# Kernel optimization log

Hardware: AMD Instinct MI355X
Metric: run time of the kernel (lower is better)

Reference implementation:

```python
import jax, jax.numpy as jnp
import numpy as np

N = 1_000_000
HID = 128

def setup_inputs() -> dict:
    key = jax.random.key(0)
    ks = jax.random.split(key, 4)
    F = jnp.eye(2, dtype=jnp.float32)[None] + 0.1 * jax.random.normal(ks[0], (N, 2, 2), dtype=jnp.float32)
    W1 = jax.random.normal(ks[1], (7, HID), dtype=jnp.float32) * (1.0 / np.sqrt(7))
    b1 = jnp.zeros((HID,), dtype=jnp.float32)
    W2 = jax.random.normal(ks[2], (HID, HID), dtype=jnp.float32) * (1.0 / np.sqrt(HID))
    b2 = jnp.zeros((HID,), dtype=jnp.float32)
    W3 = jax.random.normal(ks[3], (HID, 4), dtype=jnp.float32) * (1.0 / np.sqrt(HID))
    b3 = jnp.zeros((4,), dtype=jnp.float32)
    return {"F": F, "W1": W1, "b1": b1, "W2": W2, "b2": b2, "W3": W3, "b3": b3}

def reference(F, W1, b1, W2, b2, W3, b3):
    F = F.reshape(-1, 2, 2)                      # [N,2,2]
    U, sigma, Vh = jnp.linalg.svd(F)             # batched 2x2 SVD
    R = jnp.matmul(U, Vh)                        # rotation part, [N,2,2]
    FtF = jnp.einsum('nij,nik->njk', F, F)       # F^T F, [N,2,2]
    I = jnp.eye(2, dtype=F.dtype)
    I1 = sigma - 1.0                             # [N,2]
    I2 = (FtF - I).reshape(-1, 4)                # [N,4]
    det = F[:, 0, 0] * F[:, 1, 1] - F[:, 0, 1] * F[:, 1, 0]
    I3 = det[:, None] - 1.0                      # [N,1]
    inv = jnp.concatenate([I1, I2, I3], axis=1)  # [N,7]
    h = jax.nn.relu(inv @ W1 + b1)
    h = jax.nn.relu(h @ W2 + b2)
    x = (h @ W3 + b3).reshape(-1, 2, 2)
    x = (x + jnp.swapaxes(x, 1, 2)) * 0.5        # symmetrize
    delta_Fp = jnp.matmul(R, x)
    return delta_Fp + F
```

## Files before the change

kernel.cpp:

```cpp
#include <hip/hip_runtime.h>

typedef _Float16 f16x8 __attribute__((ext_vector_type(8)));
typedef _Float16 f16x2 __attribute__((ext_vector_type(2)));
typedef float    f32x4 __attribute__((ext_vector_type(4)));

#define MFMA(a, b, c) __builtin_amdgcn_mfma_f32_16x16x32_f16((a), (b), (c), 0, 0, 0)

__device__ inline f16x8 zero8() {
    f16x8 z;
#pragma unroll
    for (int i = 0; i < 8; ++i) z[i] = (_Float16)0.0f;
    return z;
}

__global__ __launch_bounds__(256, 1)
void DeformationCorrector_78967268704761_kernel(
        const float* __restrict__ F,
        const float* __restrict__ W1, const float* __restrict__ b1,
        const float* __restrict__ W2, const float* __restrict__ b2,
        const float* __restrict__ W3, const float* __restrict__ b3,
        float* __restrict__ out, int N)
{
    __shared__ __align__(16) _Float16 W2f[8][4][64][8];
    __shared__ __align__(16) _Float16 W1f[8][16][8];
    __shared__ __align__(16) _Float16 W3c[4][16][8];
    __shared__ __align__(16) _Float16 invL[256][8];
    __shared__ __align__(16) _Float16 scratch[4][64][40];

    const int tid  = threadIdx.x;
    const int lane = tid & 63;
    const int w    = tid >> 6;
    const int l15  = tid & 15;
    const int quad = (tid >> 4) & 3;

    for (int m = tid; m < 128 * 128; m += 256) {
        int k = m >> 7, n = m & 127;
        W2f[n >> 4][k >> 5][((k >> 3) & 3) * 16 + (n & 15)][k & 7] = (_Float16)W2[m];
    }
    for (int f = tid; f < 1024; f += 256) {
        int nt = f >> 7, n15 = (f >> 3) & 15, j = f & 7;
        W1f[nt][n15][j] = (_Float16)((j < 7) ? W1[j * 128 + nt * 16 + n15]
                                             : b1[nt * 16 + n15]);
    }
    for (int f = tid; f < 512; f += 256) {
        int s = f >> 7, idx = (f >> 3) & 15, j = f & 7;
        int q = idx >> 2, n = idx & 3;
        W3c[s][idx][j] = (_Float16)W3[(s * 32 + q * 8 + j) * 4 + n];
    }
    float b2r[8];
#pragma unroll
    for (int nt = 0; nt < 8; ++nt) b2r[nt] = b2[nt * 16 + l15];
    const float b3v = (l15 < 4) ? b3[l15] : 0.f;
    __syncthreads();

    const int ntiles = (N + 255) >> 8;
    for (int tile = blockIdx.x; tile < ntiles; tile += (int)gridDim.x) {
        const int p = tile * 256 + tid;

        float a, b, c, d;
        if (p < N) {
            const float4 f4 = *(const float4*)(F + 4ll * p);
            a = f4.x; b = f4.y; c = f4.z; d = f4.w;
        } else { a = 1.f; b = 0.f; c = 0.f; d = 1.f; }
        const float x1 = a + d, y1 = c - b, x2 = a - d, y2 = c + b;
        const float h1v = sqrtf(x1 * x1 + y1 * y1);
        const float h2v = sqrtf(x2 * x2 + y2 * y2);
        const float s1 = 0.5f * (h1v + h2v), s2 = 0.5f * (h1v - h2v);
        const float ir = 1.0f / h1v;
        const float Rc = x1 * ir, Rs = y1 * ir;
        f16x8 iv;
        iv[0] = (_Float16)(s1 - 1.f);
        iv[1] = (_Float16)(s2 - 1.f);
        iv[2] = (_Float16)(a * a + c * c - 1.f);
        const float i3 = a * b + c * d;
        iv[3] = (_Float16)i3;
        iv[4] = (_Float16)i3;
        iv[5] = (_Float16)(b * b + d * d - 1.f);
        iv[6] = (_Float16)(a * d - b * c - 1.f);
        iv[7] = (_Float16)1.0f;
        *(f16x8*)(&invL[tid][0]) = iv;

        f16x8 binv[4];
#pragma unroll
        for (int mt = 0; mt < 4; ++mt)
            binv[mt] = (quad == 0) ? *(const f16x8*)(&invL[w * 64 + mt * 16 + l15][0])
                                   : zero8();

        f32x4 acc2[8][4];
#pragma unroll
        for (int nt2 = 0; nt2 < 8; ++nt2)
#pragma unroll
            for (int mt2 = 0; mt2 < 4; ++mt2) acc2[nt2][mt2] = (f32x4){0.f, 0.f, 0.f, 0.f};

        for (int ks = 0; ks < 4; ++ks) {
#pragma unroll
            for (int h = 0; h < 2; ++h) {
                const f16x8 bw1 = (lane < 16) ? *(const f16x8*)(&W1f[2 * ks + h][l15][0])
                                              : zero8();
#pragma unroll
                for (int mt = 0; mt < 4; ++mt) {
                    f32x4 cz = {0.f, 0.f, 0.f, 0.f};
                    const f32x4 cc = MFMA(binv[mt], bw1, cz);
#pragma unroll
                    for (int r = 0; r < 4; ++r)
                        scratch[w][mt * 16 + quad * 4 + r][h * 16 + l15] =
                            (_Float16)fmaxf(cc[r], 0.f);
                }
            }
            f16x8 af[4];
#pragma unroll
            for (int mt2 = 0; mt2 < 4; ++mt2)
                af[mt2] = *(const f16x8*)(&scratch[w][mt2 * 16 + l15][quad * 8]);
#pragma unroll
            for (int nt2 = 0; nt2 < 8; ++nt2) {
                const f16x8 bf = *(const f16x8*)(&W2f[nt2][ks][lane][0]);
#pragma unroll
                for (int mt2 = 0; mt2 < 4; ++mt2)
                    acc2[nt2][mt2] = MFMA(af[mt2], bf, acc2[nt2][mt2]);
            }
        }

        f32x4 acc3[4];
#pragma unroll
        for (int mt2 = 0; mt2 < 4; ++mt2) acc3[mt2] = (f32x4){0.f, 0.f, 0.f, 0.f};

#pragma unroll
        for (int s = 0; s < 4; ++s) {
#pragma unroll
            for (int h = 0; h < 2; ++h) {
                const int nt2 = 2 * s + h;
                const float bb = b2r[nt2];
#pragma unroll
                for (int mt2 = 0; mt2 < 4; ++mt2)
#pragma unroll
                    for (int r = 0; r < 4; ++r)
                        scratch[w][mt2 * 16 + quad * 4 + r][h * 16 + l15] =
                            (_Float16)fmaxf(acc2[nt2][mt2][r] + bb, 0.f);
            }
            const f16x8 bw3 = (l15 < 4) ? *(const f16x8*)(&W3c[s][quad * 4 + l15][0])
                                        : zero8();
#pragma unroll
            for (int mt2 = 0; mt2 < 4; ++mt2) {
                const f16x8 ah = *(const f16x8*)(&scratch[w][mt2 * 16 + l15][quad * 8]);
                acc3[mt2] = MFMA(ah, bw3, acc3[mt2]);
            }
        }

        float* xf = (float*)(&scratch[w][0][0]);
#pragma unroll
        for (int mt2 = 0; mt2 < 4; ++mt2)
#pragma unroll
            for (int r = 0; r < 4; ++r)
                if (l15 < 4)
                    xf[(mt2 * 16 + quad * 4 + r) * 4 + l15] = acc3[mt2][r] + b3v;

        const float4 xv = *(const float4*)(&xf[lane * 4]);
        const float xm  = 0.5f * (xv.y + xv.z);
        const float d00 = Rc * xv.x - Rs * xm;
        const float d01 = Rc * xm   - Rs * xv.w;
        const float d10 = Rs * xv.x + Rc * xm;
        const float d11 = Rs * xm   + Rc * xv.w;
        if (p < N) {
            float4 o;
            o.x = a + d00; o.y = b + d01; o.z = c + d10; o.w = d + d11;
            *(float4*)(out + 4ll * p) = o;
        }
    }
}

extern "C" void kernel_launch(void* const* d_in, const int* in_sizes, int n_in,
                              void* d_out, int out_size, void* d_ws, size_t ws_size,
                              hipStream_t stream) {
    const float* F  = (const float*)d_in[0];
    const float* W1 = (const float*)d_in[1];
    const float* b1 = (const float*)d_in[2];
    const float* W2 = (const float*)d_in[3];
    const float* b2 = (const float*)d_in[4];
    const float* W3 = (const float*)d_in[5];
    const float* b3 = (const float*)d_in[6];
    float* out = (float*)d_out;
    const int N = in_sizes[0] / 4;
    const int ntiles = (N + 255) / 256;
    const int grid = ntiles < 1024 ? ntiles : 1024;
    DeformationCorrector_78967268704761_kernel<<<grid, 256, 0, stream>>>(
        F, W1, b1, W2, b2, W3, b3, out, N);
}
```

Measured before the change: 144.9 us.

## Keep layer-1 activations in registers via transposed MFMA and permuted W2 layout

Layer 1 now computes the transposed product (W1^T times invariants), so each lane's MFMA output fragment lands directly in the register layout needed as the A operand of layer 2. This removes the LDS round-trip for hidden layer 1 and its wave-local scratch stores and loads. W2 and W3 are repacked in shared memory with permuted k-indices to match the new fragment ordering. Layer 2 is restructured to accumulate per output-column pair and write h2 as packed half2, with a dedicated float buffer for the final outputs. It trades higher register pressure (h1 fragments held live) for fewer LDS operations.

New measurement: 162.9 us. 1.12x slower.

```diff
diff --git a/kernel.cpp b/kernel.cpp
--- a/kernel.cpp
+++ b/kernel.cpp
@@ -25,7 +25,8 @@
     __shared__ __align__(16) _Float16 W1f[8][16][8];
     __shared__ __align__(16) _Float16 W3c[4][16][8];
     __shared__ __align__(16) _Float16 invL[256][8];
-    __shared__ __align__(16) _Float16 scratch[4][64][40];
+    __shared__ __align__(16) float    xls[256][4];
+    __shared__ __align__(16) _Float16 h2s[4][64][40];
 
     const int tid  = threadIdx.x;
     const int lane = tid & 63;
@@ -34,18 +35,22 @@
     const int quad = (tid >> 4) & 3;
 
     for (int m = tid; m < 128 * 128; m += 256) {
-        int k = m >> 7, n = m & 127;
-        W2f[n >> 4][k >> 5][((k >> 3) & 3) * 16 + (n & 15)][k & 7] = (_Float16)W2[m];
+        int c = m >> 7, n = m & 127;
+        int ks = c >> 5, rem = c & 31;
+        int j = ((rem >> 4) & 1) * 4 + (rem & 3);
+        int q = (rem >> 2) & 3;
+        W2f[n >> 4][ks][q * 16 + (n & 15)][j] = (_Float16)W2[m];
     }
     for (int f = tid; f < 1024; f += 256) {
-        int nt = f >> 7, n15 = (f >> 3) & 15, j = f & 7;
-        W1f[nt][n15][j] = (_Float16)((j < 7) ? W1[j * 128 + nt * 16 + n15]
-                                             : b1[nt * 16 + n15]);
+        int mt = f >> 7, l = (f >> 3) & 15, j = f & 7;
+        int ch = mt * 16 + l;
+        W1f[mt][l][j] = (_Float16)((j < 7) ? W1[j * 128 + ch] : b1[ch]);
     }
     for (int f = tid; f < 512; f += 256) {
-        int s = f >> 7, idx = (f >> 3) & 15, j = f & 7;
-        int q = idx >> 2, n = idx & 3;
-        W3c[s][idx][j] = (_Float16)W3[(s * 32 + q * 8 + j) * 4 + n];
+        int c2 = f >> 2, n3 = f & 3;
+        int nt2 = c2 >> 4, l = c2 & 15;
+        int s = nt2 >> 1, ch = l * 2 + (nt2 & 1);
+        W3c[s][(ch >> 3) * 4 + n3][ch & 7] = (_Float16)W3[c2 * 4 + n3];
     }
     float b2r[8];
 #pragma unroll
@@ -82,79 +87,73 @@
 
         f16x8 binv[4];
 #pragma unroll
-        for (int mt = 0; mt < 4; ++mt)
-            binv[mt] = (quad == 0) ? *(const f16x8*)(&invL[w * 64 + mt * 16 + l15][0])
+        for (int nt = 0; nt < 4; ++nt)
+            binv[nt] = (quad == 0) ? *(const f16x8*)(&invL[w * 64 + nt * 16 + l15][0])
                                    : zero8();
-
-        f32x4 acc2[8][4];
+        f16x8 h1f[4][4];
 #pragma unroll
-        for (int nt2 = 0; nt2 < 8; ++nt2)
+        for (int mt = 0; mt < 8; ++mt) {
+            const f16x8 af = (quad == 0) ? *(const f16x8*)(&W1f[mt][l15][0]) : zero8();
 #pragma unroll
-            for (int mt2 = 0; mt2 < 4; ++mt2) acc2[nt2][mt2] = (f32x4){0.f, 0.f, 0.f, 0.f};
-
-        for (int ks = 0; ks < 4; ++ks) {
+            for (int nt = 0; nt < 4; ++nt) {
+                f32x4 cz = {0.f, 0.f, 0.f, 0.f};
+                const f32x4 cc = MFMA(af, binv[nt], cz);
 #pragma unroll
-            for (int h = 0; h < 2; ++h) {
-                const f16x8 bw1 = (lane < 16) ? *(const f16x8*)(&W1f[2 * ks + h][l15][0])
-                                              : zero8();
-#pragma unroll
-                for (int mt = 0; mt < 4; ++mt) {
-                    f32x4 cz = {0.f, 0.f, 0.f, 0.f};
-                    const f32x4 cc = MFMA(binv[mt], bw1, cz);
-#pragma unroll
-                    for (int r = 0; r < 4; ++r)
-                        scratch[w][mt * 16 + quad * 4 + r][h * 16 + l15] =
-                            (_Float16)fmaxf(cc[r], 0.f);
-                }
-            }
-            f16x8 af[4];
-#pragma unroll
-            for (int mt2 = 0; mt2 < 4; ++mt2)
-                af[mt2] = *(const f16x8*)(&scratch[w][mt2 * 16 + l15][quad * 8]);
-#pragma unroll
-            for (int nt2 = 0; nt2 < 8; ++nt2) {
-                const f16x8 bf = *(const f16x8*)(&W2f[nt2][ks][lane][0]);
-#pragma unroll
-                for (int mt2 = 0; mt2 < 4; ++mt2)
-                    acc2[nt2][mt2] = MFMA(af[mt2], bf, acc2[nt2][mt2]);
+                for (int r = 0; r < 4; ++r)
+                    h1f[nt][mt >> 1][(mt & 1) * 4 + r] = (_Float16)fmaxf(cc[r], 0.f);
             }
         }
 
         f32x4 acc3[4];
 #pragma unroll
-        for (int mt2 = 0; mt2 < 4; ++mt2) acc3[mt2] = (f32x4){0.f, 0.f, 0.f, 0.f};
+        for (int mt = 0; mt < 4; ++mt) acc3[mt] = (f32x4){0.f, 0.f, 0.f, 0.f};
 
 #pragma unroll
         for (int s = 0; s < 4; ++s) {
+            f32x4 a2[2][4];
+#pragma unroll
+            for (int h = 0; h < 2; ++h)
+#pragma unroll
+                for (int mt = 0; mt < 4; ++mt) a2[h][mt] = (f32x4){0.f, 0.f, 0.f, 0.f};
 #pragma unroll
             for (int h = 0; h < 2; ++h) {
                 const int nt2 = 2 * s + h;
-                const float bb = b2r[nt2];
 #pragma unroll
-                for (int mt2 = 0; mt2 < 4; ++mt2)
+                for (int ks = 0; ks < 4; ++ks) {
+                    const f16x8 bf = *(const f16x8*)(&W2f[nt2][ks][lane][0]);
 #pragma unroll
-                    for (int r = 0; r < 4; ++r)
-                        scratch[w][mt2 * 16 + quad * 4 + r][h * 16 + l15] =
-                            (_Float16)fmaxf(acc2[nt2][mt2][r] + bb, 0.f);
+                    for (int mt = 0; mt < 4; ++mt)
+                        a2[h][mt] = MFMA(h1f[mt][ks], bf, a2[h][mt]);
+                }
+            }
+            const float bb0 = b2r[2 * s], bb1 = b2r[2 * s + 1];
+#pragma unroll
+            for (int mt = 0; mt < 4; ++mt) {
+#pragma unroll
+                for (int r = 0; r < 4; ++r) {
+                    f16x2 pw;
+                    pw[0] = (_Float16)fmaxf(a2[0][mt][r] + bb0, 0.f);
+                    pw[1] = (_Float16)fmaxf(a2[1][mt][r] + bb1, 0.f);
+                    *(f16x2*)(&h2s[w][mt * 16 + quad * 4 + r][l15 * 2]) = pw;
+                }
             }
             const f16x8 bw3 = (l15 < 4) ? *(const f16x8*)(&W3c[s][quad * 4 + l15][0])
                                         : zero8();
 #pragma unroll
-            for (int mt2 = 0; mt2 < 4; ++mt2) {
-                const f16x8 ah = *(const f16x8*)(&scratch[w][mt2 * 16 + l15][quad * 8]);
-                acc3[mt2] = MFMA(ah, bw3, acc3[mt2]);
+            for (int mt = 0; mt < 4; ++mt) {
+                const f16x8 ah = *(const f16x8*)(&h2s[w][mt * 16 + l15][quad * 8]);
+                acc3[mt] = MFMA(ah, bw3, acc3[mt]);
             }
         }
 
-        float* xf = (float*)(&scratch[w][0][0]);
 #pragma unroll
-        for (int mt2 = 0; mt2 < 4; ++mt2)
+        for (int mt = 0; mt < 4; ++mt)
 #pragma unroll
             for (int r = 0; r < 4; ++r)
                 if (l15 < 4)
-                    xf[(mt2 * 16 + quad * 4 + r) * 4 + l15] = acc3[mt2][r] + b3v;
+                    xls[w * 64 + mt * 16 + quad * 4 + r][l15] = acc3[mt][r] + b3v;
 
-        const float4 xv = *(const float4*)(&xf[lane * 4]);
+        const float4 xv = *(const float4*)(&xls[w * 64 + lane][0]);
         const float xm  = 0.5f * (xv.y + xv.z);
         const float d00 = Rc * xv.x - Rs * xm;
         const float d01 = Rc * xm   - Rs * xv.w;
```
